# Performance work log

Hardware: AMD Instinct MI355X
Metric: run time of the kernel (lower is better)

The kernel has to match this reference:

```python
import jax, jax.numpy as jnp
import numpy as np

DIM = 768
HEADS = 12
HEAD_DIM = DIM // HEADS
HIDDEN = int(DIM * 4.0)
EPS = 1e-5


def layernorm(x, w, b):
    mu = jnp.mean(x, axis=-1, keepdims=True)
    var = jnp.var(x, axis=-1, keepdims=True)
    return (x - mu) * jax.lax.rsqrt(var + EPS) * w + b


def setup_inputs() -> dict:
    key = jax.random.key(0)
    ks = jax.random.split(key, 12)
    B, N = 4, 2048
    s = lambda fan_in: 1.0 / np.sqrt(fan_in)
    return {
        "x": jax.random.normal(ks[0], (B, N, DIM), dtype=jnp.float32),
        "qkv_w": jax.random.normal(ks[1], (3 * DIM, DIM), dtype=jnp.float32) * s(DIM),
        "proj_w": jax.random.normal(ks[2], (DIM, DIM), dtype=jnp.float32) * s(DIM),
        "proj_b": jnp.zeros((DIM,), dtype=jnp.float32),
        "norm1_w": jnp.ones((DIM,), dtype=jnp.float32),
        "norm1_b": jnp.zeros((DIM,), dtype=jnp.float32),
        "norm2_w": jnp.ones((DIM,), dtype=jnp.float32),
        "norm2_b": jnp.zeros((DIM,), dtype=jnp.float32),
        "fc1_w": jax.random.normal(ks[3], (HIDDEN, DIM), dtype=jnp.float32) * s(DIM),
        "fc1_b": jnp.zeros((HIDDEN,), dtype=jnp.float32),
        "fc2_w": jax.random.normal(ks[4], (DIM, HIDDEN), dtype=jnp.float32) * s(HIDDEN),
        "fc2_b": jnp.zeros((DIM,), dtype=jnp.float32),
    }


def reference(x, qkv_w, proj_w, proj_b, norm1_w, norm1_b, norm2_w, norm2_b,
              fc1_w, fc1_b, fc2_w, fc2_b):
    B, N, C = x.shape
    scale = HEAD_DIM ** -0.5
    shortcut = x
    h = layernorm(x, norm1_w, norm1_b)
    # qkv: [B, N, 3C] -> [3, B, H, N, Dh]
    qkv = (h @ qkv_w.T).reshape(B, N, 3, HEADS, HEAD_DIM)
    qkv = jnp.transpose(qkv, (2, 0, 3, 1, 4))
    q, k, v = qkv[0] * scale, qkv[1], qkv[2]
    attn = jnp.einsum("bhnd,bhmd->bhnm", q, k)
    attn = jax.nn.softmax(attn, axis=-1)
    out = jnp.einsum("bhnm,bhmd->bhnd", attn, v)
    out = jnp.transpose(out, (0, 2, 1, 3)).reshape(B, N, C)
    out = out @ proj_w.T + proj_b
    x = shortcut + out
    h2 = layernorm(x, norm2_w, norm2_b)
    mlp = jax.nn.gelu(h2 @ fc1_w.T + fc1_b, approximate=False) @ fc2_w.T + fc2_b
    return x + mlp
```

## Files before the change

### kernel.cpp

```cpp
#include <hip/hip_runtime.h>
#include <hip/hip_bf16.h>

#define SEQ   2048
#define NBAT  4
#define NH    12
#define HD    64
#define CDIM  768
#define HID   3072
#define NTOK  (SEQ*NBAT)

#define KS2 0.1803368801111244f

typedef __attribute__((ext_vector_type(8))) short short8;
typedef __attribute__((ext_vector_type(4))) float floatx4;

__device__ __forceinline__ float bf2f(unsigned short u) {
    union { unsigned int i; float f; } v; v.i = ((unsigned int)u) << 16; return v.f;
}
__device__ __forceinline__ unsigned short f2bf(float f) {
    union { float f; unsigned int i; } v; v.f = f;
    unsigned int i = v.i;
    return (unsigned short)((i + 0x7FFFu + ((i >> 16) & 1u)) >> 16);
}
__device__ __forceinline__ unsigned int fbits(float f) {
    union { float f; unsigned int i; } v; v.f = f; return v.i;
}
__device__ __forceinline__ float fast_exp2(float x) {
#if __has_builtin(__builtin_amdgcn_exp2f)
    return __builtin_amdgcn_exp2f(x);
#else
    return __expf(x * 0.69314718055994531f);
#endif
}
__device__ __forceinline__ float fast_rcp(float x) {
#if __has_builtin(__builtin_amdgcn_rcpf)
    return __builtin_amdgcn_rcpf(x);
#else
    return 1.f / x;
#endif
}
__device__ __forceinline__ float gelu_f(float v) {
    float u = 0.7978845608028654f * v * (1.f + 0.044715f * v * v);
    float e = fast_exp2(u * 2.885390081777927f);
    float th = 1.f - 2.f * fast_rcp(e + 1.f);
    return 0.5f * v * (1.f + th);
}
__device__ __forceinline__ void gload16(const unsigned short* g, unsigned short* l) {
    __builtin_amdgcn_global_load_lds(
        (const __attribute__((address_space(1))) unsigned int*)g,
        (__attribute__((address_space(3))) unsigned int*)l, 16, 0, 0);
}

__global__ __launch_bounds__(256) void cvt_all_kernel(
    const float* __restrict__ s0, const float* __restrict__ s1,
    const float* __restrict__ s2, const float* __restrict__ s3,
    unsigned short* __restrict__ d0, unsigned short* __restrict__ d1,
    unsigned short* __restrict__ d2, unsigned short* __restrict__ d3)
{
    int blk = blockIdx.x;
    const float* src; unsigned short* dst; int off;
    if (blk < 1728)      { src = s0; dst = d0; off = blk; }
    else if (blk < 2304) { src = s1; dst = d1; off = blk - 1728; }
    else if (blk < 4608) { src = s2; dst = d2; off = blk - 2304; }
    else                 { src = s3; dst = d3; off = blk - 4608; }
    int i = (off * 256 + threadIdx.x) * 4;
    float4 f = *(const float4*)(src + i);
    ushort4 o;
    o.x = f2bf(f.x); o.y = f2bf(f.y); o.z = f2bf(f.z); o.w = f2bf(f.w);
    *(ushort4*)(dst + i) = o;
}

__global__ __launch_bounds__(256) void ln_kernel(
    const float* __restrict__ x, const float* __restrict__ w,
    const float* __restrict__ b, unsigned short* __restrict__ y)
{
    int row  = blockIdx.x * 4 + (threadIdx.x >> 6);
    int lane = threadIdx.x & 63;
    const float4* xr = (const float4*)(x + (size_t)row * CDIM);
    float4 v[3];
    float s = 0.f, sq = 0.f;
#pragma unroll
    for (int i = 0; i < 3; i++) {
        float4 f = xr[lane + i * 64];
        v[i] = f;
        s  += (f.x + f.y) + (f.z + f.w);
        sq += (f.x * f.x + f.y * f.y) + (f.z * f.z + f.w * f.w);
    }
#pragma unroll
    for (int o = 32; o > 0; o >>= 1) {
        s  += __shfl_xor(s,  o, 64);
        sq += __shfl_xor(sq, o, 64);
    }
    float mean = s * (1.f / CDIM);
    float var  = sq * (1.f / CDIM) - mean * mean;
    float rstd = rsqrtf(var + 1e-5f);
    const float4* w4 = (const float4*)w;
    const float4* b4 = (const float4*)b;
    ushort4* y4 = (ushort4*)(y + (size_t)row * CDIM);
#pragma unroll
    for (int i = 0; i < 3; i++) {
        int c = lane + i * 64;
        float4 wf = w4[c], bf_ = b4[c];
        ushort4 o;
        o.x = f2bf((v[i].x - mean) * rstd * wf.x + bf_.x);
        o.y = f2bf((v[i].y - mean) * rstd * wf.y + bf_.y);
        o.z = f2bf((v[i].z - mean) * rstd * wf.z + bf_.z);
        o.w = f2bf((v[i].w - mean) * rstd * wf.w + bf_.w);
        y4[c] = o;
    }
}

#define BK 64

template<int ACT, int OUT32, int TM>
__global__ __launch_bounds__(256) void gemm_bt(
    const unsigned short* __restrict__ A, const unsigned short* __restrict__ W,
    const float* __restrict__ bias, const float* __restrict__ res,
    void* __restrict__ Cv, int M, int N, int K, int scol, float scale)
{
    constexpr int MT   = TM / 32;
    constexpr int ISSA = TM / 32;
    __shared__ __align__(16) unsigned short As[TM * BK];
    __shared__ __align__(16) unsigned short Bs[128 * BK];
    int tid  = threadIdx.x;
    int wave = tid >> 6, lane = tid & 63;
    int wr = wave >> 1, wc = wave & 1;
    int quad = lane >> 4, l15 = lane & 15;
    int m0 = blockIdx.x * TM, n0 = blockIdx.y * 128;

    int r8 = lane >> 3;
    int kc = (lane & 7) ^ r8;
    const unsigned short* Ag = A + (size_t)(m0 + wave * (TM / 4) + r8) * K + kc * 8;
    const unsigned short* Wg = W + (size_t)(n0 + wave * 32 + r8) * K + kc * 8;
    unsigned short* AsW = As + wave * (TM / 4) * BK;
    unsigned short* BsW = Bs + wave * 32 * BK;

    floatx4 acc[MT][4];
    floatx4 fz = {0.f, 0.f, 0.f, 0.f};
#pragma unroll
    for (int i = 0; i < MT; i++)
#pragma unroll
        for (int j = 0; j < 4; j++) acc[i][j] = fz;

    int sw = l15 & 7;
    for (int k0 = 0; k0 < K; k0 += BK) {
        __syncthreads();
#pragma unroll
        for (int j = 0; j < ISSA; j++)
            gload16(Ag + (size_t)(8 * j) * K + k0, AsW + j * 512);
#pragma unroll
        for (int j = 0; j < 4; j++)
            gload16(Wg + (size_t)(8 * j) * K + k0, BsW + j * 512);
        __syncthreads();

#pragma unroll
        for (int s = 0; s < 2; s++) {
            short8 af[MT], bfg[4];
            int ko = ((s * 4 + quad) ^ sw) * 8;
#pragma unroll
            for (int mt = 0; mt < MT; mt++)
                af[mt] = *(const short8*)(As + (wr * (TM / 2) + mt * 16 + l15) * BK + ko);
#pragma unroll
            for (int nt = 0; nt < 4; nt++)
                bfg[nt] = *(const short8*)(Bs + (wc * 64 + nt * 16 + l15) * BK + ko);
#pragma unroll
            for (int mt = 0; mt < MT; mt++)
#pragma unroll
                for (int nt = 0; nt < 4; nt++)
                    acc[mt][nt] = __builtin_amdgcn_mfma_f32_16x16x32_bf16(
                        af[mt], bfg[nt], acc[mt][nt], 0, 0, 0);
        }
    }

#pragma unroll
    for (int mt = 0; mt < MT; mt++) {
#pragma unroll
        for (int nt = 0; nt < 4; nt++) {
            int col = n0 + wc * 64 + nt * 16 + l15;
            float bv = bias ? bias[col] : 0.f;
            float cs = (col < scol) ? scale : 1.f;
#pragma unroll
            for (int r = 0; r < 4; r++) {
                int row = m0 + wr * (TM / 2) + mt * 16 + quad * 4 + r;
                size_t idx = (size_t)row * N + col;
                float v = acc[mt][nt][r] + bv;
                if (res) v += res[idx];
                if (ACT == 1) v = gelu_f(v);
                v *= cs;
                if (OUT32) ((float*)Cv)[idx] = v;
                else       ((unsigned short*)Cv)[idx] = f2bf(v);
            }
        }
    }
}

__global__ __launch_bounds__(256) void attn_kernel(
    const unsigned short* __restrict__ qkv, unsigned short* __restrict__ out)
{
    __shared__ __align__(16) unsigned short Ks[2][64 * 64];
    __shared__ __align__(16) unsigned short Vt[2][64 * 72];
    __shared__ __align__(16) unsigned short Ps[4][2][16 * 72];

    int tid  = threadIdx.x;
    int wave = tid >> 6, lane = tid & 63;
    int quad = lane >> 4, l15 = lane & 15;
    int bh = blockIdx.y;
    int b  = bh / NH, h = bh % NH;
    size_t base = (size_t)b * SEQ * 2304 + h * 64;
    int qbase = blockIdx.x * 128 + wave * 32;

    short8 bq[2][2];
#pragma unroll
    for (int qh = 0; qh < 2; qh++)
#pragma unroll
        for (int kk = 0; kk < 2; kk++)
            bq[qh][kk] = *(const short8*)(qkv + base +
                (size_t)(qbase + qh * 16 + l15) * 2304 + kk * 32 + quad * 8);

    floatx4 o[2][4];
    floatx4 fz = {0.f, 0.f, 0.f, 0.f};
#pragma unroll
    for (int qh = 0; qh < 2; qh++)
#pragma unroll
        for (int dg = 0; dg < 4; dg++) o[qh][dg] = fz;
    float m2[2] = {-3e38f, -3e38f};
    float ls[2] = {0.f, 0.f};

    const unsigned short* kg = qkv + base + 768 +
        (size_t)(wave * 16 + (lane >> 3)) * 2304 + (((lane & 7) ^ ((lane >> 3) & 7)) * 8);
    const unsigned short* vptr = qkv + base + 1536;
    int vj  = tid & 31;
    int vd8 = wave * 16 + ((tid >> 5) & 1) * 8;
    int sw  = l15 & 7;

    gload16(kg, &Ks[0][wave * 1024]);
    gload16(kg + (size_t)8 * 2304, &Ks[0][wave * 1024 + 512]);
    {
        uint4 v0v = *(const uint4*)(vptr + (size_t)(2 * vj)     * 2304 + vd8);
        uint4 v1v = *(const uint4*)(vptr + (size_t)(2 * vj + 1) * 2304 + vd8);
        union { uint4 q; unsigned short u[8]; } u0, u1;
        u0.q = v0v; u1.q = v1v;
#pragma unroll
        for (int i = 0; i < 8; i++) {
            unsigned int w = (unsigned int)u0.u[i] | ((unsigned int)u1.u[i] << 16);
            *(unsigned int*)(&Vt[0][(vd8 + i) * 72 + 2 * vj]) = w;
        }
    }
    __syncthreads();

    for (int t = 0; t < SEQ / 64; t++) {
        int cur = t & 1, nxt = cur ^ 1;
        bool more = (t + 1 < SEQ / 64);
        uint4 v0v, v1v;
        if (more) {
            const unsigned short* kg2 = kg + (size_t)(t + 1) * 64 * 2304;
            gload16(kg2, &Ks[nxt][wave * 1024]);
            gload16(kg2 + (size_t)8 * 2304, &Ks[nxt][wave * 1024 + 512]);
            int kt = (t + 1) * 64;
            v0v = *(const uint4*)(vptr + (size_t)(kt + 2 * vj)     * 2304 + vd8);
            v1v = *(const uint4*)(vptr + (size_t)(kt + 2 * vj + 1) * 2304 + vd8);
        }

        floatx4 st[2][4];
#pragma unroll
        for (int ts = 0; ts < 4; ts++) {
            short8 ak0 = *(const short8*)(&Ks[cur][(ts * 16 + l15) * 64 + (((0 * 4 + quad) ^ sw) * 8)]);
            short8 ak1 = *(const short8*)(&Ks[cur][(ts * 16 + l15) * 64 + (((1 * 4 + quad) ^ sw) * 8)]);
            floatx4 s0 = __builtin_amdgcn_mfma_f32_16x16x32_bf16(ak0, bq[0][0], fz, 0, 0, 0);
            s0 = __builtin_amdgcn_mfma_f32_16x16x32_bf16(ak1, bq[0][1], s0, 0, 0, 0);
            floatx4 s1 = __builtin_amdgcn_mfma_f32_16x16x32_bf16(ak0, bq[1][0], fz, 0, 0, 0);
            s1 = __builtin_amdgcn_mfma_f32_16x16x32_bf16(ak1, bq[1][1], s1, 0, 0, 0);
            st[0][ts] = s0; st[1][ts] = s1;
        }

#pragma unroll
        for (int qh = 0; qh < 2; qh++) {
            float tmax = st[qh][0][0];
#pragma unroll
            for (int ts = 0; ts < 4; ts++)
#pragma unroll
                for (int r = 0; r < 4; r++) tmax = fmaxf(tmax, st[qh][ts][r]);
            tmax = fmaxf(tmax, __shfl_xor(tmax, 16, 64));
            tmax = fmaxf(tmax, __shfl_xor(tmax, 32, 64));
            if (tmax > m2[qh]) {
                float alpha = fast_exp2(m2[qh] - tmax);
                m2[qh] = tmax;
                ls[qh] *= alpha;
#pragma unroll
                for (int dg = 0; dg < 4; dg++)
#pragma unroll
                    for (int r = 0; r < 4; r++) o[qh][dg][r] *= alpha;
            }
            float mm = m2[qh];
            float psum = 0.f;
#pragma unroll
            for (int ts = 0; ts < 4; ts++) {
                float p0 = fast_exp2(st[qh][ts][0] - mm);
                float p1 = fast_exp2(st[qh][ts][1] - mm);
                float p2 = fast_exp2(st[qh][ts][2] - mm);
                float p3 = fast_exp2(st[qh][ts][3] - mm);
                psum += (p0 + p1) + (p2 + p3);
                unsigned int w01 = __builtin_amdgcn_perm(fbits(p1), fbits(p0), 0x07060302);
                unsigned int w23 = __builtin_amdgcn_perm(fbits(p3), fbits(p2), 0x07060302);
                uint2 wv; wv.x = w01; wv.y = w23;
                *(uint2*)(&Ps[wave][qh][l15 * 72 + ts * 16 + quad * 4]) = wv;
            }
            ls[qh] += psum;
        }

#pragma unroll
        for (int hk = 0; hk < 2; hk++) {
            short8 bp0 = *(const short8*)(&Ps[wave][0][l15 * 72 + hk * 32 + quad * 8]);
            short8 bp1 = *(const short8*)(&Ps[wave][1][l15 * 72 + hk * 32 + quad * 8]);
#pragma unroll
            for (int dg = 0; dg < 4; dg++) {
                short8 av = *(const short8*)(&Vt[cur][(dg * 16 + l15) * 72 + hk * 32 + quad * 8]);
                o[0][dg] = __builtin_amdgcn_mfma_f32_16x16x32_bf16(av, bp0, o[0][dg], 0, 0, 0);
                o[1][dg] = __builtin_amdgcn_mfma_f32_16x16x32_bf16(av, bp1, o[1][dg], 0, 0, 0);
            }
        }

        if (more) {
            union { uint4 q; unsigned short u[8]; } u0, u1;
            u0.q = v0v; u1.q = v1v;
#pragma unroll
            for (int i = 0; i < 8; i++) {
                unsigned int w = (unsigned int)u0.u[i] | ((unsigned int)u1.u[i] << 16);
                *(unsigned int*)(&Vt[nxt][(vd8 + i) * 72 + 2 * vj]) = w;
            }
        }
        __syncthreads();
    }

#pragma unroll
    for (int qh = 0; qh < 2; qh++) {
        float l = ls[qh];
        l += __shfl_xor(l, 16, 64);
        l += __shfl_xor(l, 32, 64);
        float inv = 1.f / l;
        size_t orow = ((size_t)b * SEQ + qbase + qh * 16 + l15) * CDIM + h * 64;
#pragma unroll
        for (int dg = 0; dg < 4; dg++) {
            unsigned int u0 = (unsigned int)f2bf(o[qh][dg][0] * inv) | ((unsigned int)f2bf(o[qh][dg][1] * inv) << 16);
            unsigned int u1 = (unsigned int)f2bf(o[qh][dg][2] * inv) | ((unsigned int)f2bf(o[qh][dg][3] * inv) << 16);
            uint2 wv; wv.x = u0; wv.y = u1;
            *(uint2*)((unsigned short*)out + orow + dg * 16 + quad * 4) = wv;
        }
    }
}

extern "C" void kernel_launch(void* const* d_in, const int* in_sizes, int n_in,
                              void* d_out, int out_size, void* d_ws, size_t ws_size,
                              hipStream_t stream)
{
    const float* x      = (const float*)d_in[0];
    const float* qkv_w  = (const float*)d_in[1];
    const float* proj_w = (const float*)d_in[2];
    const float* proj_b = (const float*)d_in[3];
    const float* n1w    = (const float*)d_in[4];
    const float* n1b    = (const float*)d_in[5];
    const float* n2w    = (const float*)d_in[6];
    const float* n2b    = (const float*)d_in[7];
    const float* fc1w   = (const float*)d_in[8];
    const float* fc1b   = (const float*)d_in[9];
    const float* fc2w   = (const float*)d_in[10];
    const float* fc2b   = (const float*)d_in[11];
    float* out = (float*)d_out;

    unsigned short* ws = (unsigned short*)d_ws;
    unsigned short* wq = ws;
    unsigned short* wp = wq + 1769472;
    unsigned short* w1 = wp + 589824;
    unsigned short* w2 = w1 + 2359296;
    unsigned short* h    = w2 + 2359296;
    unsigned short* qkv  = h + 6291456;
    unsigned short* attn = qkv + 18874368;
    unsigned short* a    = qkv;

    dim3 blk(256);
    cvt_all_kernel<<<6912, blk, 0, stream>>>(qkv_w, proj_w, fc1w, fc2w, wq, wp, w1, w2);

    ln_kernel<<<NTOK / 4, blk, 0, stream>>>(x, n1w, n1b, h);
    gemm_bt<0, 0, 128><<<dim3(NTOK / 128, 2304 / 128), blk, 0, stream>>>(
        h, wq, nullptr, nullptr, qkv, NTOK, 2304, 768, 768, KS2);
    attn_kernel<<<dim3(SEQ / 128, NBAT * NH), blk, 0, stream>>>(qkv, attn);
    gemm_bt<0, 1, 64><<<dim3(NTOK / 64, 768 / 128), blk, 0, stream>>>(
        attn, wp, proj_b, x, out, NTOK, 768, 768, 0, 1.f);
    ln_kernel<<<NTOK / 4, blk, 0, stream>>>(out, n2w, n2b, h);
    gemm_bt<1, 0, 128><<<dim3(NTOK / 128, 3072 / 128), blk, 0, stream>>>(
        h, w1, fc1b, nullptr, a, NTOK, 3072, 768, 0, 1.f);
    gemm_bt<0, 1, 64><<<dim3(NTOK / 64, 768 / 128), blk, 0, stream>>>(
        a, w2, fc2b, out, out, NTOK, 768, 3072, 0, 1.f);
}
```

Baseline: 385.1 us.

## Keep attention probabilities in registers via permlane swaps instead of LDS round-trip

The attention kernel no longer writes the softmax probabilities to a per-wave LDS buffer and reads them back as MFMA operands. It rearranges them in registers using v_permlane32_swap/v_permlane16_swap. It also adds a lazy rescale that only updates the running max when it grows by more than a threshold, wraps the MFMA sections in s_setprio, and sets launch bounds to 4 waves per SIMD. These changes target LDS traffic, waitcnt stalls and rescale work, at the cost of more register pressure and reliance on gfx950-specific permlane instructions.

```diff
diff --git a/kernel.cpp b/kernel.cpp
--- a/kernel.cpp
+++ b/kernel.cpp
@@ -49,6 +49,12 @@
     __builtin_amdgcn_global_load_lds(
         (const __attribute__((address_space(1))) unsigned int*)g,
         (__attribute__((address_space(3))) unsigned int*)l, 16, 0, 0);
+}
+__device__ __forceinline__ void pl32_swap(unsigned int& x, unsigned int& y) {
+    asm("v_permlane32_swap_b32 %0, %1" : "+v"(x), "+v"(y));
+}
+__device__ __forceinline__ void pl16_swap(unsigned int& x, unsigned int& y) {
+    asm("v_permlane16_swap_b32 %0, %1" : "+v"(x), "+v"(y));
 }
 
 __global__ __launch_bounds__(256) void cvt_all_kernel(
@@ -194,12 +200,11 @@
     }
 }
 
-__global__ __launch_bounds__(256) void attn_kernel(
+__global__ __launch_bounds__(256, 4) void attn_kernel(
     const unsigned short* __restrict__ qkv, unsigned short* __restrict__ out)
 {
     __shared__ __align__(16) unsigned short Ks[2][64 * 64];
     __shared__ __align__(16) unsigned short Vt[2][64 * 72];
-    __shared__ __align__(16) unsigned short Ps[4][2][16 * 72];
 
     int tid  = threadIdx.x;
     int wave = tid >> 6, lane = tid & 63;
@@ -262,6 +267,7 @@
         }
 
         floatx4 st[2][4];
+        __builtin_amdgcn_s_setprio(1);
 #pragma unroll
         for (int ts = 0; ts < 4; ts++) {
             short8 ak0 = *(const short8*)(&Ks[cur][(ts * 16 + l15) * 64 + (((0 * 4 + quad) ^ sw) * 8)]);
@@ -272,19 +278,23 @@
             s1 = __builtin_amdgcn_mfma_f32_16x16x32_bf16(ak1, bq[1][1], s1, 0, 0, 0);
             st[0][ts] = s0; st[1][ts] = s1;
         }
-
+        __builtin_amdgcn_s_setprio(0);
+
+        unsigned int pw[2][4][2];
 #pragma unroll
         for (int qh = 0; qh < 2; qh++) {
-            float tmax = st[qh][0][0];
+            float tm[4];
 #pragma unroll
             for (int ts = 0; ts < 4; ts++)
-#pragma unroll
-                for (int r = 0; r < 4; r++) tmax = fmaxf(tmax, st[qh][ts][r]);
+                tm[ts] = fmaxf(fmaxf(st[qh][ts][0], st[qh][ts][1]),
+                               fmaxf(st[qh][ts][2], st[qh][ts][3]));
+            float tmax = fmaxf(fmaxf(tm[0], tm[1]), fmaxf(tm[2], tm[3]));
             tmax = fmaxf(tmax, __shfl_xor(tmax, 16, 64));
             tmax = fmaxf(tmax, __shfl_xor(tmax, 32, 64));
-            if (tmax > m2[qh]) {
-                float alpha = fast_exp2(m2[qh] - tmax);
-                m2[qh] = tmax;
+            if (!__all(tmax <= m2[qh] + 8.f)) {
+                float nm = fmaxf(m2[qh], tmax);
+                float alpha = fast_exp2(m2[qh] - nm);
+                m2[qh] = nm;
                 ls[qh] *= alpha;
 #pragma unroll
                 for (int dg = 0; dg < 4; dg++)
@@ -300,24 +310,33 @@
                 float p2 = fast_exp2(st[qh][ts][2] - mm);
                 float p3 = fast_exp2(st[qh][ts][3] - mm);
                 psum += (p0 + p1) + (p2 + p3);
-                unsigned int w01 = __builtin_amdgcn_perm(fbits(p1), fbits(p0), 0x07060302);
-                unsigned int w23 = __builtin_amdgcn_perm(fbits(p3), fbits(p2), 0x07060302);
-                uint2 wv; wv.x = w01; wv.y = w23;
-                *(uint2*)(&Ps[wave][qh][l15 * 72 + ts * 16 + quad * 4]) = wv;
+                pw[qh][ts][0] = __builtin_amdgcn_perm(fbits(p1), fbits(p0), 0x07060302);
+                pw[qh][ts][1] = __builtin_amdgcn_perm(fbits(p3), fbits(p2), 0x07060302);
             }
             ls[qh] += psum;
         }
 
 #pragma unroll
         for (int hk = 0; hk < 2; hk++) {
-            short8 bp0 = *(const short8*)(&Ps[wave][0][l15 * 72 + hk * 32 + quad * 8]);
-            short8 bp1 = *(const short8*)(&Ps[wave][1][l15 * 72 + hk * 32 + quad * 8]);
+            short8 bp[2];
+#pragma unroll
+            for (int qh = 0; qh < 2; qh++) {
+                unsigned int x0 = pw[qh][2 * hk][0], y0 = pw[qh][2 * hk + 1][0];
+                unsigned int x1 = pw[qh][2 * hk][1], y1 = pw[qh][2 * hk + 1][1];
+                pl32_swap(x0, y0); pl16_swap(x0, y0);
+                pl32_swap(x1, y1); pl16_swap(x1, y1);
+                union { unsigned int u[4]; short8 s; } f;
+                f.u[0] = x0; f.u[1] = x1; f.u[2] = y0; f.u[3] = y1;
+                bp[qh] = f.s;
+            }
+            __builtin_amdgcn_s_setprio(1);
 #pragma unroll
             for (int dg = 0; dg < 4; dg++) {
                 short8 av = *(const short8*)(&Vt[cur][(dg * 16 + l15) * 72 + hk * 32 + quad * 8]);
-                o[0][dg] = __builtin_amdgcn_mfma_f32_16x16x32_bf16(av, bp0, o[0][dg], 0, 0, 0);
-                o[1][dg] = __builtin_amdgcn_mfma_f32_16x16x32_bf16(av, bp1, o[1][dg], 0, 0, 0);
-            }
+                o[0][dg] = __builtin_amdgcn_mfma_f32_16x16x32_bf16(av, bp[0], o[0][dg], 0, 0, 0);
+                o[1][dg] = __builtin_amdgcn_mfma_f32_16x16x32_bf16(av, bp[1], o[1][dg], 0, 0, 0);
+            }
+            __builtin_amdgcn_s_setprio(0);
         }
 
         if (more) {
```

New measurement: 395.8 us. 1.03x slower.
